# Kernel optimization log

Hardware: AMD Instinct MI355X
Metric: run time of the kernel (lower is better)

The kernel has to match this reference:

```python
import jax, jax.numpy as jnp
import numpy as np

N_NODES, EMB, HID, HEADS, E = 50000, 128, 64, 3, 800000


def setup_inputs() -> dict:
    key = jax.random.key(0)
    ks = jax.random.split(key, 12)
    HC = HEADS * HID
    return {
        "edge_index": jax.random.randint(ks[0], (2, E), 0, N_NODES),
        "edge_attr": jax.random.uniform(ks[1], (E, 1), dtype=jnp.float32),
        "path_emb": jax.random.normal(ks[2], (N_NODES, EMB), dtype=jnp.float32) * (2.0 / EMB) ** 0.5,
        "sim_w": jnp.ones((1,), dtype=jnp.float32),
        "Wl": jax.random.normal(ks[3], (HC, EMB), dtype=jnp.float32) / np.sqrt(EMB),
        "bl": jnp.zeros((HC,), dtype=jnp.float32),
        "Wr": jax.random.normal(ks[4], (HC, EMB), dtype=jnp.float32) / np.sqrt(EMB),
        "br": jnp.zeros((HC,), dtype=jnp.float32),
        "We": jax.random.normal(ks[5], (HC, 1), dtype=jnp.float32),
        "att": jax.random.normal(ks[6], (1, HEADS, HID), dtype=jnp.float32) / np.sqrt(HID),
        "bias_gnn": jnp.zeros((HID,), dtype=jnp.float32),
        "Wout": jax.random.normal(ks[7], (1, HID), dtype=jnp.float32) / np.sqrt(HID),
        "bout": jnp.zeros((1,), dtype=jnp.float32),
    }


def reference(edge_index, edge_attr, path_emb, sim_w, Wl, bl, Wr, br, We, att, bias_gnn, Wout, bout):
    # SimFusionModule: softmax-weighted combination over sim channels -> [E, 1]
    w = jax.nn.softmax(sim_w, axis=0)
    fused = (edge_attr * w).sum(axis=1, keepdims=True)  # [E,1]

    # GATv2Conv (concat=False, no self loops, edge_dim=1)
    xl = (path_emb @ Wl.T + bl).reshape(-1, HEADS, HID)  # source transform [N,H,C]
    xr = (path_emb @ Wr.T + br).reshape(-1, HEADS, HID)  # target transform [N,H,C]
    src, dst = edge_index[0], edge_index[1]
    xj = xl[src]                                          # [E,H,C] gathered source
    xi = xr[dst]                                          # [E,H,C] gathered target
    ef = (fused @ We.T).reshape(-1, HEADS, HID)           # [E,H,C] edge features
    m = xj + xi + ef
    a = (jax.nn.leaky_relu(m, 0.2) * att).sum(-1)         # [E,H] attention logits

    # segment softmax over incoming edges of each destination node
    amax = jax.ops.segment_max(a, dst, num_segments=N_NODES)
    aexp = jnp.exp(a - amax[dst])
    asum = jax.ops.segment_sum(aexp, dst, num_segments=N_NODES)
    alpha = aexp / asum[dst]                              # [E,H]

    out = jax.ops.segment_sum(alpha[:, :, None] * xj, dst, num_segments=N_NODES)  # [N,H,C]
    out = out.mean(axis=1) + bias_gnn                     # concat=False -> head mean, + bias

    scores = (out @ Wout.T + bout).squeeze()              # [N]
    return jax.nn.softmax(scores, axis=0)
```

## Files before the change

### kernel.cpp

```cpp
#include <hip/hip_runtime.h>
#include <cfloat>
#include <cmath>

#define NHEADS 3
#define HIDC   64
#define HCC    192
#define EMBC   128
#define WCOLS  384
#define CAP    1280

typedef unsigned short bhalf;
typedef __attribute__((ext_vector_type(8))) short bf16x8;
typedef __attribute__((ext_vector_type(4))) float f32x4;
typedef __attribute__((ext_vector_type(2))) float f32x2;

__device__ __forceinline__ unsigned f2bf(float f) {
  unsigned u = __float_as_uint(f);
  return (u + 0x7FFFu + ((u >> 16) & 1u)) >> 16;
}

__global__ __launch_bounds__(256) void prep_kernel(
    const float* __restrict__ Wl, const float* __restrict__ Wr,
    const float* __restrict__ bl, const float* __restrict__ br,
    const float* __restrict__ Wout, const float* __restrict__ We,
    const float* __restrict__ att,
    bhalf* __restrict__ Wb, float* __restrict__ vh, float* __restrict__ b16,
    float* __restrict__ We16, float* __restrict__ att16, float* __restrict__ ch,
    unsigned* __restrict__ cur, float* __restrict__ sumexp, int NB)
{
  const int BASE = WCOLS * EMBC;
  int gt = blockIdx.x * 256 + threadIdx.x;
  if (gt < BASE) {
    int c = gt >> 7, k = gt & 127;
    float v = (c < HCC) ? Wl[c * EMBC + k] : Wr[(c - HCC) * EMBC + k];
    Wb[gt] = (bhalf)f2bf(v);
  } else if (gt < BASE + 384) {
    int i = gt - BASE;
    int h = i >> 7, k = i & 127;
    float s = 0.f;
    for (int c = 0; c < HIDC; ++c)
      s += Wout[c] * Wl[(h * HIDC + c) * EMBC + k];
    vh[i] = s;
  } else if (gt < BASE + 768) {
    int c = gt - BASE - 384;
    b16[c] = 16.f * ((c < HCC) ? bl[c] : br[c - HCC]);
  } else if (gt < BASE + 960) {
    int c = gt - BASE - 768;
    We16[c] = 16.f * We[c];
  } else if (gt < BASE + 1152) {
    int c = gt - BASE - 960;
    att16[c] = att[c] * (1.f / 16.f);
  } else if (gt < BASE + 1155) {
    int h = gt - BASE - 1152;
    float s = 0.f;
    for (int c = 0; c < HIDC; ++c) s += bl[h * HIDC + c] * Wout[c];
    ch[h] = s;
  } else if (gt < BASE + 1155 + NB) {
    int b = gt - BASE - 1155;
    cur[b * 16] = (unsigned)(b * CAP);
  } else if (gt == BASE + 1155 + NB) {
    *sumexp = 0.f;
  }
}

__global__ __launch_bounds__(256, 4) void gemm_kernel(
    const float* __restrict__ pe, const bhalf* __restrict__ Wb,
    const float* __restrict__ b16, const float* __restrict__ vh,
    const float* __restrict__ ch,
    unsigned char* __restrict__ xl8, unsigned char* __restrict__ xr8,
    float* __restrict__ pj, int N)
{
  __shared__ bhalf Ws[192 * 64];
  const int tid  = threadIdx.x;
  const int w    = tid >> 6;
  const int lane = tid & 63;
  const int m    = lane & 15;
  const int q    = lane >> 4;
  const int nb   = blockIdx.x >> 1;
  const int half = blockIdx.x & 1;
  const int n0   = nb * 64;
  const int node = n0 + w * 16 + m;
  const size_t prow = (size_t)(node < N ? node : N - 1) * EMBC;

  bf16x8 pfrag[4];
  float pjp[3] = {0.f, 0.f, 0.f};
  #pragma unroll
  for (int kt = 0; kt < 4; ++kt) {
    const float* p = pe + prow + kt * 32 + q * 8;
    float4 x = *(const float4*)p;
    float4 y = *(const float4*)(p + 4);
    if (half == 0) {
      #pragma unroll
      for (int h = 0; h < 3; ++h) {
        const float* v = vh + h * EMBC + kt * 32 + q * 8;
        float4 va = *(const float4*)v;
        float4 vb = *(const float4*)(v + 4);
        pjp[h] += x.x*va.x + x.y*va.y + x.z*va.z + x.w*va.w
                + y.x*vb.x + y.y*vb.y + y.z*vb.z + y.w*vb.w;
      }
    }
    union { bf16x8 v; unsigned u[4]; } uu;
    uu.u[0] = (__float_as_uint(x.x) >> 16) | (__float_as_uint(x.y) & 0xFFFF0000u);
    uu.u[1] = (__float_as_uint(x.z) >> 16) | (__float_as_uint(x.w) & 0xFFFF0000u);
    uu.u[2] = (__float_as_uint(y.x) >> 16) | (__float_as_uint(y.y) & 0xFFFF0000u);
    uu.u[3] = (__float_as_uint(y.z) >> 16) | (__float_as_uint(y.w) & 0xFFFF0000u);
    pfrag[kt] = uu.v;
  }

  f32x4 acc[12];
  #pragma unroll
  for (int t = 0; t < 12; ++t) acc[t] = (f32x4){0.f, 0.f, 0.f, 0.f};

  for (int kh = 0; kh < 2; ++kh) {
    __syncthreads();
    for (int f = tid; f < 192 * 8; f += 256) {
      int cc = f >> 3, s = f & 7;
      uint4 v = *(const uint4*)(Wb + (size_t)(half * HCC + cc) * EMBC + kh * 64 + s * 8);
      *(uint4*)(Ws + cc * 64 + ((s ^ (cc & 7)) * 8)) = v;
    }
    __syncthreads();
    #pragma unroll
    for (int kt2 = 0; kt2 < 2; ++kt2) {
      #pragma unroll
      for (int t = 0; t < 12; ++t) {
        bf16x8 wf = *(const bf16x8*)(Ws + (t * 16 + m) * 64 + (((kt2 << 2) + q) ^ (m & 7)) * 8);
        acc[t] = __builtin_amdgcn_mfma_f32_16x16x32_bf16(wf, pfrag[kh * 2 + kt2], acc[t], 0, 0, 0);
      }
    }
  }

  if (half == 0) {
    #pragma unroll
    for (int h = 0; h < 3; ++h) {
      pjp[h] += __shfl_xor(pjp[h], 16);
      pjp[h] += __shfl_xor(pjp[h], 32);
    }
    if (q == 0 && node < N) {
      pj[node * 3 + 0] = pjp[0] + ch[0];
      pj[node * 3 + 1] = pjp[1] + ch[1];
      pj[node * 3 + 2] = pjp[2] + ch[2];
    }
  }

  if (node < N) {
    unsigned char* xo = half ? xr8 : xl8;
    #pragma unroll
    for (int t = 0; t < 12; ++t) {
      int col = t * 16 + q * 4;
      float4 b = *(const float4*)(b16 + half * HCC + col);
      float r0 = fmaf(acc[t][0], 16.f, b.x);
      float r1 = fmaf(acc[t][1], 16.f, b.y);
      float r2 = fmaf(acc[t][2], 16.f, b.z);
      float r3 = fmaf(acc[t][3], 16.f, b.w);
      int p = 0;
      p = __builtin_amdgcn_cvt_pk_fp8_f32(r0, r1, p, false);
      p = __builtin_amdgcn_cvt_pk_fp8_f32(r2, r3, p, true);
      *(unsigned*)(xo + (size_t)node * HCC + col) = (unsigned)p;
    }
  }
}

#define SCH 4096
__global__ __launch_bounds__(256) void scatter_kernel(
    const int* __restrict__ ei, const float* __restrict__ ea,
    uint2* __restrict__ eb, unsigned* __restrict__ cur, int E, int NB)
{
  __shared__ unsigned lh[800], lbase[800];
  int tid = threadIdx.x;
  int base = blockIdx.x * SCH;
  for (int i = tid; i < NB; i += 256) lh[i] = 0;
  __syncthreads();
  #pragma unroll 4
  for (int i = 0; i < SCH / 256; ++i) {
    int e = base + i * 256 + tid;
    if (e < E) atomicAdd(&lh[ei[E + e] >> 6], 1u);
  }
  __syncthreads();
  for (int i = tid; i < NB; i += 256) {
    unsigned c = lh[i];
    lbase[i] = c ? atomicAdd(&cur[i * 16], c) : 0u;
    lh[i] = 0;
  }
  __syncthreads();
  #pragma unroll 4
  for (int i = 0; i < SCH / 256; ++i) {
    int e = base + i * 256 + tid;
    if (e < E) {
      int src = ei[e], dst = ei[E + e];
      int bin = dst >> 6;
      unsigned slot = lbase[bin] + atomicAdd(&lh[bin], 1u);
      uint2 rec;
      rec.x = (unsigned)src | ((unsigned)dst << 16);
      rec.y = __float_as_uint(ea[e]);
      eb[slot] = rec;
    }
  }
}

#define EPG 5
#define GPW 4
#define WCHUNK (EPG * GPW)
__global__ __launch_bounds__(512, 4) void edge_kernel(
    const uint2* __restrict__ eb,
    const unsigned char* __restrict__ xl8, const unsigned char* __restrict__ xr8,
    const float* __restrict__ pj, const float* __restrict__ We16,
    const float* __restrict__ att16, const unsigned* __restrict__ cur,
    float* __restrict__ sumexp, float* __restrict__ out, int N)
{
  __shared__ uint4 xrs[64][12];
  __shared__ float facc[64][8];
  const int tid  = threadIdx.x;
  const int w    = tid >> 6;
  const int lane = tid & 63;
  const int j = lane / 12;
  const int c = lane % 12;
  const bool act = lane < 60;
  const int b = blockIdx.x;
  const int n0 = b << 6;
  const int start = b * CAP;
  const int end   = (int)cur[b * 16];

  for (int i = tid; i < 768; i += 512) {
    int row = i / 12, sl = i % 12;
    int nn = n0 + row; if (nn >= N) nn = N - 1;
    xrs[row][sl] = *(const uint4*)(xr8 + (size_t)nn * HCC + sl * 16);
  }
  for (int i = tid; i < 512; i += 512) ((float*)facc)[i] = 0.f;

  float4 we[4], at[4];
  #pragma unroll
  for (int i = 0; i < 4; ++i) {
    we[i] = *(const float4*)(We16 + c * 16 + i * 4);
    at[i] = *(const float4*)(att16 + c * 16 + i * 4);
  }
  __syncthreads();

  const int wstart = start + w * WCHUNK;
  uint2 rec[GPW];
  #pragma unroll
  for (int g = 0; g < GPW; ++g) {
    int e = wstart + g * EPG + j;
    rec[g] = eb[e < end ? e : start];
  }

  for (int cb = wstart; cb < end; cb += 8 * WCHUNK) {
    int srcs[GPW], dsts[GPW]; float eavs[GPW];
    #pragma unroll
    for (int g = 0; g < GPW; ++g) {
      srcs[g] = (int)(rec[g].x & 0xFFFFu);
      dsts[g] = (int)(rec[g].x >> 16);
      eavs[g] = __uint_as_float(rec[g].y);
    }
    uint4 ul[GPW]; float pjv[GPW];
    #pragma unroll
    for (int g = 0; g < GPW; ++g)
      ul[g] = *(const uint4*)(xl8 + (size_t)srcs[g] * HCC + c * 16);
    #pragma unroll
    for (int g = 0; g < GPW; ++g)
      pjv[g] = pj[srcs[g] * 3 + (c >> 2)];
    uint4 ur[GPW];
    #pragma unroll
    for (int g = 0; g < GPW; ++g)
      ur[g] = xrs[dsts[g] & 63][c];

    int nxt = cb + 8 * WCHUNK;
    #pragma unroll
    for (int g = 0; g < GPW; ++g) {
      int e = nxt + g * EPG + j;
      rec[g] = eb[(e < end) ? e : start];
    }

    #pragma unroll
    for (int g = 0; g < GPW; ++g) {
      const unsigned* ulp = &ul[g].x;
      const unsigned* urp = &ur[g].x;
      float sc = 0.f;
      #pragma unroll
      for (int i = 0; i < 4; ++i) {
        f32x2 l0 = __builtin_amdgcn_cvt_pk_f32_fp8(ulp[i], false);
        f32x2 l1 = __builtin_amdgcn_cvt_pk_f32_fp8(ulp[i], true);
        f32x2 r0 = __builtin_amdgcn_cvt_pk_f32_fp8(urp[i], false);
        f32x2 r1 = __builtin_amdgcn_cvt_pk_f32_fp8(urp[i], true);
        float m0 = l0.x + r0.x + eavs[g] * we[i].x;
        float m1 = l0.y + r0.y + eavs[g] * we[i].y;
        float m2 = l1.x + r1.x + eavs[g] * we[i].z;
        float m3 = l1.y + r1.y + eavs[g] * we[i].w;
        sc += fmaxf(m0, 0.2f * m0) * at[i].x
            + fmaxf(m1, 0.2f * m1) * at[i].y
            + fmaxf(m2, 0.2f * m2) * at[i].z
            + fmaxf(m3, 0.2f * m3) * at[i].w;
      }
      sc += __shfl_xor(sc, 1);
      sc += __shfl_xor(sc, 2);
      bool ve = act && (cb + g * EPG + j < end);
      if (ve && (c & 3) == 0) {
        int h = c >> 2;
        int ld = dsts[g] & 63;
        float ex = __expf(sc);
        atomicAdd(&facc[ld][h], ex);
        atomicAdd(&facc[ld][3 + h], ex * pjv[g]);
      }
    }
  }
  __syncthreads();

  if (tid < 64) {
    int n = n0 + tid;
    float e = 0.f;
    if (n < N) {
      float accs = 0.f;
      #pragma unroll
      for (int h = 0; h < 3; ++h) {
        float d = facc[tid][h];
        if (d > 0.f) accs += facc[tid][3 + h] / d;
      }
      e = expf(accs * (1.f / 3.f));
      out[n] = e;
    }
    #pragma unroll
    for (int o = 32; o; o >>= 1) e += __shfl_xor(e, o);
    if (tid == 0) atomicAdd(sumexp, e);
  }
}

__global__ __launch_bounds__(256) void norm_kernel(
    float* __restrict__ out, const float* __restrict__ sumexp, int N)
{
  int n = blockIdx.x * 256 + threadIdx.x;
  if (n < N) out[n] /= *sumexp;
}

extern "C" void kernel_launch(void* const* d_in, const int* in_sizes, int n_in,
                              void* d_out, int out_size, void* d_ws, size_t ws_size,
                              hipStream_t stream) {
  const int*   ei   = (const int*)  d_in[0];
  const float* ea   = (const float*)d_in[1];
  const float* pe   = (const float*)d_in[2];
  const float* Wl   = (const float*)d_in[4];
  const float* bl   = (const float*)d_in[5];
  const float* Wr   = (const float*)d_in[6];
  const float* br   = (const float*)d_in[7];
  const float* We   = (const float*)d_in[8];
  const float* att  = (const float*)d_in[9];
  const float* Wout = (const float*)d_in[11];

  const int E = in_sizes[0] / 2;
  const int N = in_sizes[2] / EMBC;
  const int NB = (N + 63) >> 6;
  float* out = (float*)d_out;

  float* ws       = (float*)d_ws;
  float* sumexp   = ws;
  unsigned* cur   = (unsigned*)(ws + 16);
  float* pj       = ws + 16 + (size_t)NB * 16;
  float* vh       = pj + (size_t)3 * N;
  float* b16      = vh + 384;
  float* We16     = b16 + 384;
  float* att16    = We16 + 192;
  float* ch       = att16 + 192;
  bhalf* Wb       = (bhalf*)(ch + 16);
  unsigned char* xl8 = (unsigned char*)(Wb + (size_t)WCOLS * EMBC);
  unsigned char* xr8 = xl8 + (size_t)N * HCC;
  uint2* eb       = (uint2*)(xr8 + (size_t)N * HCC);

  const int BASE = WCOLS * EMBC;
  prep_kernel  <<<(BASE + 1155 + NB + 1 + 255) / 256, 256, 0, stream>>>(
      Wl, Wr, bl, br, Wout, We, att, Wb, vh, b16, We16, att16, ch,
      cur, sumexp, NB);
  gemm_kernel  <<<NB * 2, 256, 0, stream>>>(pe, Wb, b16, vh, ch, xl8, xr8, pj, N);
  scatter_kernel<<<(E + SCH - 1) / SCH, 256, 0, stream>>>(ei, ea, eb, cur, E, NB);
  edge_kernel  <<<NB, 512, 0, stream>>>(eb, xl8, xr8, pj, We16, att16, cur,
                                        sumexp, out, N);
  norm_kernel  <<<(N + 255) / 256, 256, 0, stream>>>(out, sumexp, N);
}
```

Baseline: 204.5 us.

## Split each destination bucket across four edge blocks with separate finalize kernel

The edge kernel now launches four 256-thread blocks per 64-node bucket instead of one 512-thread block, with each block handling an interleaved slice of the bucket's edges. Each block writes its partial shared-memory accumulators to global memory, and a new finalize kernel sums the partials, computes node scores and accumulates the softmax denominator. This is meant to raise occupancy and parallelism over the ~782 buckets. The cost is that every block reloads the xr tile, there is extra global traffic for partials, and one more launch. Other changes: the shared xr tile is padded to 13 columns to avoid bank conflicts, and the scatter chunk shrinks to 1024 edges so more blocks run.

```diff
diff --git a/kernel.cpp b/kernel.cpp
--- a/kernel.cpp
+++ b/kernel.cpp
@@ -8,6 +8,7 @@
 #define EMBC   128
 #define WCOLS  384
 #define CAP    1280
+#define SPLIT  4
 
 typedef unsigned short bhalf;
 typedef __attribute__((ext_vector_type(8))) short bf16x8;
@@ -160,7 +161,7 @@
   }
 }
 
-#define SCH 4096
+#define SCH 1024
 __global__ __launch_bounds__(256) void scatter_kernel(
     const int* __restrict__ ei, const float* __restrict__ ea,
     uint2* __restrict__ eb, unsigned* __restrict__ cur, int E, int NB)
@@ -200,14 +201,14 @@
 #define EPG 5
 #define GPW 4
 #define WCHUNK (EPG * GPW)
-__global__ __launch_bounds__(512, 4) void edge_kernel(
+__global__ __launch_bounds__(256, 4) void edge_kernel(
     const uint2* __restrict__ eb,
     const unsigned char* __restrict__ xl8, const unsigned char* __restrict__ xr8,
     const float* __restrict__ pj, const float* __restrict__ We16,
     const float* __restrict__ att16, const unsigned* __restrict__ cur,
-    float* __restrict__ sumexp, float* __restrict__ out, int N)
-{
-  __shared__ uint4 xrs[64][12];
+    float* __restrict__ pfacc, int N)
+{
+  __shared__ uint4 xrs[64][13];
   __shared__ float facc[64][8];
   const int tid  = threadIdx.x;
   const int w    = tid >> 6;
@@ -215,17 +216,19 @@
   const int j = lane / 12;
   const int c = lane % 12;
   const bool act = lane < 60;
-  const int b = blockIdx.x;
-  const int n0 = b << 6;
-  const int start = b * CAP;
-  const int end   = (int)cur[b * 16];
-
-  for (int i = tid; i < 768; i += 512) {
-    int row = i / 12, sl = i % 12;
+  const int blk    = blockIdx.x;
+  const int bucket = blk >> 2;
+  const int sl     = blk & 3;
+  const int n0 = bucket << 6;
+  const int start = bucket * CAP;
+  const int end   = (int)cur[bucket * 16];
+
+  for (int i = tid; i < 768; i += 256) {
+    int row = i / 12, slot = i % 12;
     int nn = n0 + row; if (nn >= N) nn = N - 1;
-    xrs[row][sl] = *(const uint4*)(xr8 + (size_t)nn * HCC + sl * 16);
-  }
-  for (int i = tid; i < 512; i += 512) ((float*)facc)[i] = 0.f;
+    xrs[row][slot] = *(const uint4*)(xr8 + (size_t)nn * HCC + slot * 16);
+  }
+  for (int i = tid; i < 512; i += 256) ((float*)facc)[i] = 0.f;
 
   float4 we[4], at[4];
   #pragma unroll
@@ -235,7 +238,8 @@
   }
   __syncthreads();
 
-  const int wstart = start + w * WCHUNK;
+  const int gw = sl * 4 + w;
+  const int wstart = start + gw * WCHUNK;
   uint2 rec[GPW];
   #pragma unroll
   for (int g = 0; g < GPW; ++g) {
@@ -243,7 +247,7 @@
     rec[g] = eb[e < end ? e : start];
   }
 
-  for (int cb = wstart; cb < end; cb += 8 * WCHUNK) {
+  for (int cb = wstart; cb < end; cb += 16 * WCHUNK) {
     int srcs[GPW], dsts[GPW]; float eavs[GPW];
     #pragma unroll
     for (int g = 0; g < GPW; ++g) {
@@ -263,7 +267,7 @@
     for (int g = 0; g < GPW; ++g)
       ur[g] = xrs[dsts[g] & 63][c];
 
-    int nxt = cb + 8 * WCHUNK;
+    int nxt = cb + 16 * WCHUNK;
     #pragma unroll
     for (int g = 0; g < GPW; ++g) {
       int e = nxt + g * EPG + j;
@@ -304,23 +308,41 @@
   }
   __syncthreads();
 
-  if (tid < 64) {
-    int n = n0 + tid;
-    float e = 0.f;
-    if (n < N) {
-      float accs = 0.f;
-      #pragma unroll
-      for (int h = 0; h < 3; ++h) {
-        float d = facc[tid][h];
-        if (d > 0.f) accs += facc[tid][3 + h] / d;
-      }
-      e = expf(accs * (1.f / 3.f));
-      out[n] = e;
-    }
-    #pragma unroll
-    for (int o = 32; o; o >>= 1) e += __shfl_xor(e, o);
-    if (tid == 0) atomicAdd(sumexp, e);
-  }
+  for (int i = tid; i < 512; i += 256)
+    pfacc[(size_t)blk * 512 + i] = ((float*)facc)[i];
+}
+
+__global__ __launch_bounds__(256) void finalize_kernel(
+    const float* __restrict__ pfacc, float* __restrict__ sumexp,
+    float* __restrict__ out, int N)
+{
+  int n = blockIdx.x * 256 + threadIdx.x;
+  int t = threadIdx.x;
+  float e = 0.f;
+  if (n < N) {
+    int bucket = n >> 6, ld = n & 63;
+    float a0 = 0.f, a1 = 0.f, a2 = 0.f, m0 = 0.f, m1 = 0.f, m2 = 0.f;
+    #pragma unroll
+    for (int s = 0; s < SPLIT; ++s) {
+      const float* p = pfacc + ((size_t)(bucket * SPLIT + s) * 512) + ld * 8;
+      a0 += p[0]; a1 += p[1]; a2 += p[2];
+      m0 += p[3]; m1 += p[4]; m2 += p[5];
+    }
+    float accs = 0.f;
+    if (a0 > 0.f) accs += m0 / a0;
+    if (a1 > 0.f) accs += m1 / a1;
+    if (a2 > 0.f) accs += m2 / a2;
+    e = expf(accs * (1.f / 3.f));
+    out[n] = e;
+  }
+  __shared__ float red[256];
+  red[t] = e;
+  __syncthreads();
+  for (int w = 128; w; w >>= 1) {
+    if (t < w) red[t] += red[t + w];
+    __syncthreads();
+  }
+  if (t == 0) atomicAdd(sumexp, red[0]);
 }
 
 __global__ __launch_bounds__(256) void norm_kernel(
@@ -356,12 +378,13 @@
   float* vh       = pj + (size_t)3 * N;
   float* b16      = vh + 384;
   float* We16     = b16 + 384;
-  float* att16    = We16 + 192;
+  float* att16   = We16 + 192;
   float* ch       = att16 + 192;
   bhalf* Wb       = (bhalf*)(ch + 16);
   unsigned char* xl8 = (unsigned char*)(Wb + (size_t)WCOLS * EMBC);
   unsigned char* xr8 = xl8 + (size_t)N * HCC;
   uint2* eb       = (uint2*)(xr8 + (size_t)N * HCC);
+  float* pfacc    = (float*)(eb + (size_t)NB * CAP);
 
   const int BASE = WCOLS * EMBC;
   prep_kernel  <<<(BASE + 1155 + NB + 1 + 255) / 256, 256, 0, stream>>>(
@@ -369,7 +392,8 @@
       cur, sumexp, NB);
   gemm_kernel  <<<NB * 2, 256, 0, stream>>>(pe, Wb, b16, vh, ch, xl8, xr8, pj, N);
   scatter_kernel<<<(E + SCH - 1) / SCH, 256, 0, stream>>>(ei, ea, eb, cur, E, NB);
-  edge_kernel  <<<NB, 512, 0, stream>>>(eb, xl8, xr8, pj, We16, att16, cur,
-                                        sumexp, out, N);
+  edge_kernel  <<<NB * SPLIT, 256, 0, stream>>>(eb, xl8, xr8, pj, We16, att16,
+                                                cur, pfacc, N);
+  finalize_kernel<<<(N + 255) / 256, 256, 0, stream>>>(pfacc, sumexp, out, N);
   norm_kernel  <<<(N + 255) / 256, 256, 0, stream>>>(out, sumexp, N);
 }
```

After: 229.5 us. 1.12x slower.

## Store node features as fp16, use packed fp16 math, fuse gemm with scatter

Applied to the files above, without the earlier changes.

Replaces the fp8-with-scaling storage of the projected node features with fp16 and rewrites the edge attention loop to use packed half2 adds, max and fdot2. The gemm and edge-bucketing scatter kernels are merged into one launch, with blocks chosen by index and LDS shared through a union. The aim is to cut conversion instructions and one launch, and to let the gemm and scatter work overlap. In exchange, the source feature gathers and the xr tile in LDS are twice as large, which adds memory traffic in the gather-bound edge kernel.

```diff
diff --git a/kernel.cpp b/kernel.cpp
--- a/kernel.cpp
+++ b/kernel.cpp
@@ -8,15 +8,20 @@
 #define EMBC   128
 #define WCOLS  384
 #define CAP    1280
+#define SCH    4096
 
 typedef unsigned short bhalf;
+typedef __fp16 half_t;
+typedef __attribute__((ext_vector_type(2))) __fp16 h2;
 typedef __attribute__((ext_vector_type(8))) short bf16x8;
 typedef __attribute__((ext_vector_type(4))) float f32x4;
-typedef __attribute__((ext_vector_type(2))) float f32x2;
 
 __device__ __forceinline__ unsigned f2bf(float f) {
   unsigned u = __float_as_uint(f);
   return (u + 0x7FFFu + ((u >> 16) & 1u)) >> 16;
+}
+__device__ __forceinline__ unsigned h2bits(h2 v) {
+  union { h2 h; unsigned u; } cv; cv.h = v; return cv.u;
 }
 
 __global__ __launch_bounds__(256) void prep_kernel(
@@ -24,9 +29,10 @@
     const float* __restrict__ bl, const float* __restrict__ br,
     const float* __restrict__ Wout, const float* __restrict__ We,
     const float* __restrict__ att,
-    bhalf* __restrict__ Wb, float* __restrict__ vh, float* __restrict__ b16,
-    float* __restrict__ We16, float* __restrict__ att16, float* __restrict__ ch,
-    unsigned* __restrict__ cur, float* __restrict__ sumexp, int NB)
+    bhalf* __restrict__ Wb, float* __restrict__ vh, float* __restrict__ bfl,
+    unsigned* __restrict__ weh, unsigned* __restrict__ atth,
+    float* __restrict__ ch, unsigned* __restrict__ cur,
+    float* __restrict__ sumexp, int NB)
 {
   const int BASE = WCOLS * EMBC;
   int gt = blockIdx.x * 256 + threadIdx.x;
@@ -43,156 +49,151 @@
     vh[i] = s;
   } else if (gt < BASE + 768) {
     int c = gt - BASE - 384;
-    b16[c] = 16.f * ((c < HCC) ? bl[c] : br[c - HCC]);
+    bfl[c] = (c < HCC) ? bl[c] : br[c - HCC];
+  } else if (gt < BASE + 864) {
+    int i = gt - BASE - 768;
+    weh[i] = h2bits(__builtin_amdgcn_cvt_pkrtz(We[2 * i], We[2 * i + 1]));
   } else if (gt < BASE + 960) {
-    int c = gt - BASE - 768;
-    We16[c] = 16.f * We[c];
-  } else if (gt < BASE + 1152) {
-    int c = gt - BASE - 960;
-    att16[c] = att[c] * (1.f / 16.f);
-  } else if (gt < BASE + 1155) {
-    int h = gt - BASE - 1152;
+    int i = gt - BASE - 864;
+    atth[i] = h2bits(__builtin_amdgcn_cvt_pkrtz(att[2 * i], att[2 * i + 1]));
+  } else if (gt < BASE + 963) {
+    int h = gt - BASE - 960;
     float s = 0.f;
     for (int c = 0; c < HIDC; ++c) s += bl[h * HIDC + c] * Wout[c];
     ch[h] = s;
-  } else if (gt < BASE + 1155 + NB) {
-    int b = gt - BASE - 1155;
+  } else if (gt < BASE + 963 + NB) {
+    int b = gt - BASE - 963;
     cur[b * 16] = (unsigned)(b * CAP);
-  } else if (gt == BASE + 1155 + NB) {
+  } else if (gt == BASE + 963 + NB) {
     *sumexp = 0.f;
   }
 }
 
-__global__ __launch_bounds__(256, 4) void gemm_kernel(
+__global__ __launch_bounds__(256, 4) void gemmscatter_kernel(
     const float* __restrict__ pe, const bhalf* __restrict__ Wb,
-    const float* __restrict__ b16, const float* __restrict__ vh,
+    const float* __restrict__ bfl, const float* __restrict__ vh,
     const float* __restrict__ ch,
-    unsigned char* __restrict__ xl8, unsigned char* __restrict__ xr8,
-    float* __restrict__ pj, int N)
+    half_t* __restrict__ xlh, half_t* __restrict__ xrh,
+    float* __restrict__ pj, int N,
+    const int* __restrict__ ei, const float* __restrict__ ea,
+    uint2* __restrict__ eb, unsigned* __restrict__ cur, int E, int NB2)
 {
-  __shared__ bhalf Ws[192 * 64];
-  const int tid  = threadIdx.x;
-  const int w    = tid >> 6;
-  const int lane = tid & 63;
-  const int m    = lane & 15;
-  const int q    = lane >> 4;
-  const int nb   = blockIdx.x >> 1;
-  const int half = blockIdx.x & 1;
-  const int n0   = nb * 64;
-  const int node = n0 + w * 16 + m;
-  const size_t prow = (size_t)(node < N ? node : N - 1) * EMBC;
-
-  bf16x8 pfrag[4];
-  float pjp[3] = {0.f, 0.f, 0.f};
-  #pragma unroll
-  for (int kt = 0; kt < 4; ++kt) {
-    const float* p = pe + prow + kt * 32 + q * 8;
-    float4 x = *(const float4*)p;
-    float4 y = *(const float4*)(p + 4);
+  __shared__ union {
+    bhalf Ws[192 * 64];
+    struct { unsigned lh[800]; unsigned lbase[800]; } s;
+  } sm;
+  const int tid = threadIdx.x;
+
+  if ((int)blockIdx.x < NB2) {
+    const int w    = tid >> 6;
+    const int lane = tid & 63;
+    const int m    = lane & 15;
+    const int q    = lane >> 4;
+    const int nb   = blockIdx.x >> 1;
+    const int half = blockIdx.x & 1;
+    const int node = nb * 64 + w * 16 + m;
+    const size_t prow = (size_t)(node < N ? node : N - 1) * EMBC;
+
+    bf16x8 pfrag[4];
+    float pjp[3] = {0.f, 0.f, 0.f};
+    #pragma unroll
+    for (int kt = 0; kt < 4; ++kt) {
+      const float* p = pe + prow + kt * 32 + q * 8;
+      float4 x = *(const float4*)p;
+      float4 y = *(const float4*)(p + 4);
+      if (half == 0) {
+        #pragma unroll
+        for (int h = 0; h < 3; ++h) {
+          const float* v = vh + h * EMBC + kt * 32 + q * 8;
+          float4 va = *(const float4*)v;
+          float4 vb = *(const float4*)(v + 4);
+          pjp[h] += x.x*va.x + x.y*va.y + x.z*va.z + x.w*va.w
+                  + y.x*vb.x + y.y*vb.y + y.z*vb.z + y.w*vb.w;
+        }
+      }
+      union { bf16x8 v; unsigned u[4]; } uu;
+      uu.u[0] = (__float_as_uint(x.x) >> 16) | (__float_as_uint(x.y) & 0xFFFF0000u);
+      uu.u[1] = (__float_as_uint(x.z) >> 16) | (__float_as_uint(x.w) & 0xFFFF0000u);
+      uu.u[2] = (__float_as_uint(y.x) >> 16) | (__float_as_uint(y.y) & 0xFFFF0000u);
+      uu.u[3] = (__float_as_uint(y.z) >> 16) | (__float_as_uint(y.w) & 0xFFFF0000u);
+      pfrag[kt] = uu.v;
+    }
+
+    f32x4 acc[12];
+    #pragma unroll
+    for (int t = 0; t < 12; ++t) acc[t] = (f32x4){0.f, 0.f, 0.f, 0.f};
+
+    for (int kh = 0; kh < 2; ++kh) {
+      __syncthreads();
+      for (int f = tid; f < 192 * 8; f += 256) {
+        int cc = f >> 3, s = f & 7;
+        uint4 v = *(const uint4*)(Wb + (size_t)(half * HCC + cc) * EMBC + kh * 64 + s * 8);
+        *(uint4*)(sm.Ws + cc * 64 + ((s ^ (cc & 7)) * 8)) = v;
+      }
+      __syncthreads();
+      #pragma unroll
+      for (int kt2 = 0; kt2 < 2; ++kt2) {
+        #pragma unroll
+        for (int t = 0; t < 12; ++t) {
+          bf16x8 wf = *(const bf16x8*)(sm.Ws + (t * 16 + m) * 64 + (((kt2 << 2) + q) ^ (m & 7)) * 8);
+          acc[t] = __builtin_amdgcn_mfma_f32_16x16x32_bf16(wf, pfrag[kh * 2 + kt2], acc[t], 0, 0, 0);
+        }
+      }
+    }
+
     if (half == 0) {
       #pragma unroll
       for (int h = 0; h < 3; ++h) {
-        const float* v = vh + h * EMBC + kt * 32 + q * 8;
-        float4 va = *(const float4*)v;
-        float4 vb = *(const float4*)(v + 4);
-        pjp[h] += x.x*va.x + x.y*va.y + x.z*va.z + x.w*va.w
-                + y.x*vb.x + y.y*vb.y + y.z*vb.z + y.w*vb.w;
-      }
-    }
-    union { bf16x8 v; unsigned u[4]; } uu;
-    uu.u[0] = (__float_as_uint(x.x) >> 16) | (__float_as_uint(x.y) & 0xFFFF0000u);
-    uu.u[1] = (__float_as_uint(x.z) >> 16) | (__float_as_uint(x.w) & 0xFFFF0000u);
-    uu.u[2] = (__float_as_uint(y.x) >> 16) | (__float_as_uint(y.y) & 0xFFFF0000u);
-    uu.u[3] = (__float_as_uint(y.z) >> 16) | (__float_as_uint(y.w) & 0xFFFF0000u);
-    pfrag[kt] = uu.v;
-  }
-
-  f32x4 acc[12];
-  #pragma unroll
-  for (int t = 0; t < 12; ++t) acc[t] = (f32x4){0.f, 0.f, 0.f, 0.f};
-
-  for (int kh = 0; kh < 2; ++kh) {
+        pjp[h] += __shfl_xor(pjp[h], 16);
+        pjp[h] += __shfl_xor(pjp[h], 32);
+      }
+      if (q == 0 && node < N) {
+        pj[node * 3 + 0] = pjp[0] + ch[0];
+        pj[node * 3 + 1] = pjp[1] + ch[1];
+        pj[node * 3 + 2] = pjp[2] + ch[2];
+      }
+    }
+
+    if (node < N) {
+      half_t* xo = half ? xrh : xlh;
+      #pragma unroll
+      for (int t = 0; t < 12; ++t) {
+        int col = t * 16 + q * 4;
+        float4 b = *(const float4*)(bfl + half * HCC + col);
+        h2 pa = __builtin_amdgcn_cvt_pkrtz(acc[t][0] + b.x, acc[t][1] + b.y);
+        h2 pb = __builtin_amdgcn_cvt_pkrtz(acc[t][2] + b.z, acc[t][3] + b.w);
+        uint2 st; st.x = h2bits(pa); st.y = h2bits(pb);
+        *(uint2*)(xo + (size_t)node * HCC + col) = st;
+      }
+    }
+  } else {
+    const int base = (blockIdx.x - NB2) * SCH;
+    for (int i = tid; i < 800; i += 256) sm.s.lh[i] = 0;
     __syncthreads();
-    for (int f = tid; f < 192 * 8; f += 256) {
-      int cc = f >> 3, s = f & 7;
-      uint4 v = *(const uint4*)(Wb + (size_t)(half * HCC + cc) * EMBC + kh * 64 + s * 8);
-      *(uint4*)(Ws + cc * 64 + ((s ^ (cc & 7)) * 8)) = v;
+    #pragma unroll 4
+    for (int i = 0; i < SCH / 256; ++i) {
+      int e = base + i * 256 + tid;
+      if (e < E) atomicAdd(&sm.s.lh[ei[E + e] >> 6], 1u);
     }
     __syncthreads();
-    #pragma unroll
-    for (int kt2 = 0; kt2 < 2; ++kt2) {
-      #pragma unroll
-      for (int t = 0; t < 12; ++t) {
-        bf16x8 wf = *(const bf16x8*)(Ws + (t * 16 + m) * 64 + (((kt2 << 2) + q) ^ (m & 7)) * 8);
-        acc[t] = __builtin_amdgcn_mfma_f32_16x16x32_bf16(wf, pfrag[kh * 2 + kt2], acc[t], 0, 0, 0);
-      }
-    }
-  }
-
-  if (half == 0) {
-    #pragma unroll
-    for (int h = 0; h < 3; ++h) {
-      pjp[h] += __shfl_xor(pjp[h], 16);
-      pjp[h] += __shfl_xor(pjp[h], 32);
-    }
-    if (q == 0 && node < N) {
-      pj[node * 3 + 0] = pjp[0] + ch[0];
-      pj[node * 3 + 1] = pjp[1] + ch[1];
-      pj[node * 3 + 2] = pjp[2] + ch[2];
-    }
-  }
-
-  if (node < N) {
-    unsigned char* xo = half ? xr8 : xl8;
-    #pragma unroll
-    for (int t = 0; t < 12; ++t) {
-      int col = t * 16 + q * 4;
-      float4 b = *(const float4*)(b16 + half * HCC + col);
-      float r0 = fmaf(acc[t][0], 16.f, b.x);
-      float r1 = fmaf(acc[t][1], 16.f, b.y);
-      float r2 = fmaf(acc[t][2], 16.f, b.z);
-      float r3 = fmaf(acc[t][3], 16.f, b.w);
-      int p = 0;
-      p = __builtin_amdgcn_cvt_pk_fp8_f32(r0, r1, p, false);
-      p = __builtin_amdgcn_cvt_pk_fp8_f32(r2, r3, p, true);
-      *(unsigned*)(xo + (size_t)node * HCC + col) = (unsigned)p;
-    }
-  }
-}
-
-#define SCH 4096
-__global__ __launch_bounds__(256) void scatter_kernel(
-    const int* __restrict__ ei, const float* __restrict__ ea,
-    uint2* __restrict__ eb, unsigned* __restrict__ cur, int E, int NB)
-{
-  __shared__ unsigned lh[800], lbase[800];
-  int tid = threadIdx.x;
-  int base = blockIdx.x * SCH;
-  for (int i = tid; i < NB; i += 256) lh[i] = 0;
-  __syncthreads();
-  #pragma unroll 4
-  for (int i = 0; i < SCH / 256; ++i) {
-    int e = base + i * 256 + tid;
-    if (e < E) atomicAdd(&lh[ei[E + e] >> 6], 1u);
-  }
-  __syncthreads();
-  for (int i = tid; i < NB; i += 256) {
-    unsigned c = lh[i];
-    lbase[i] = c ? atomicAdd(&cur[i * 16], c) : 0u;
-    lh[i] = 0;
-  }
-  __syncthreads();
-  #pragma unroll 4
-  for (int i = 0; i < SCH / 256; ++i) {
-    int e = base + i * 256 + tid;
-    if (e < E) {
-      int src = ei[e], dst = ei[E + e];
-      int bin = dst >> 6;
-      unsigned slot = lbase[bin] + atomicAdd(&lh[bin], 1u);
-      uint2 rec;
-      rec.x = (unsigned)src | ((unsigned)dst << 16);
-      rec.y = __float_as_uint(ea[e]);
-      eb[slot] = rec;
+    for (int i = tid; i < 800; i += 256) {
+      unsigned c = sm.s.lh[i];
+      sm.s.lbase[i] = c ? atomicAdd(&cur[i * 16], c) : 0u;
+      sm.s.lh[i] = 0;
+    }
+    __syncthreads();
+    #pragma unroll 4
+    for (int i = 0; i < SCH / 256; ++i) {
+      int e = base + i * 256 + tid;
+      if (e < E) {
+        int src = ei[e], dst = ei[E + e];
+        int bin = dst >> 6;
+        unsigned slot = sm.s.lbase[bin] + atomicAdd(&sm.s.lh[bin], 1u);
+        uint2 rec;
+        rec.x = (unsigned)src | ((unsigned)dst << 16);
+        rec.y = __float_as_uint(ea[e]);
+        eb[slot] = rec;
+      }
     }
   }
 }
@@ -202,12 +203,12 @@
 #define WCHUNK (EPG * GPW)
 __global__ __launch_bounds__(512, 4) void edge_kernel(
     const uint2* __restrict__ eb,
-    const unsigned char* __restrict__ xl8, const unsigned char* __restrict__ xr8,
-    const float* __restrict__ pj, const float* __restrict__ We16,
-    const float* __restrict__ att16, const unsigned* __restrict__ cur,
+    const half_t* __restrict__ xlh, const half_t* __restrict__ xrh,
+    const float* __restrict__ pj, const unsigned* __restrict__ weh,
+    const unsigned* __restrict__ atth, const unsigned* __restrict__ cur,
     float* __restrict__ sumexp, float* __restrict__ out, int N)
 {
-  __shared__ uint4 xrs[64][12];
+  __shared__ uint4 xrs[64][25];
   __shared__ float facc[64][8];
   const int tid  = threadIdx.x;
   const int w    = tid >> 6;
@@ -220,19 +221,20 @@
   const int start = b * CAP;
   const int end   = (int)cur[b * 16];
 
-  for (int i = tid; i < 768; i += 512) {
-    int row = i / 12, sl = i % 12;
+  for (int i = tid; i < 64 * 24; i += 512) {
+    int row = i / 24, sl = i % 24;
     int nn = n0 + row; if (nn >= N) nn = N - 1;
-    xrs[row][sl] = *(const uint4*)(xr8 + (size_t)nn * HCC + sl * 16);
-  }
-  for (int i = tid; i < 512; i += 512) ((float*)facc)[i] = 0.f;
-
-  float4 we[4], at[4];
-  #pragma unroll
-  for (int i = 0; i < 4; ++i) {
-    we[i] = *(const float4*)(We16 + c * 16 + i * 4);
-    at[i] = *(const float4*)(att16 + c * 16 + i * 4);
-  }
+    xrs[row][sl] = *(const uint4*)(xrh + (size_t)nn * HCC + sl * 8);
+  }
+  if (tid < 512) ((float*)facc)[tid] = 0.f;
+
+  union U8 { uint4 u[2]; h2 h[8]; };
+  U8 we, at;
+  we.u[0] = *(const uint4*)(weh + c * 8);
+  we.u[1] = *(const uint4*)(weh + c * 8 + 4);
+  at.u[0] = *(const uint4*)(atth + c * 8);
+  at.u[1] = *(const uint4*)(atth + c * 8 + 4);
+  const h2 c02 = {(__fp16)0.2f, (__fp16)0.2f};
   __syncthreads();
 
   const int wstart = start + w * WCHUNK;
@@ -251,17 +253,17 @@
       dsts[g] = (int)(rec[g].x >> 16);
       eavs[g] = __uint_as_float(rec[g].y);
     }
-    uint4 ul[GPW]; float pjv[GPW];
-    #pragma unroll
-    for (int g = 0; g < GPW; ++g)
-      ul[g] = *(const uint4*)(xl8 + (size_t)srcs[g] * HCC + c * 16);
+    union U8x { uint4 u[2]; h2 h[8]; };
+    U8x ul[GPW]; float pjv[GPW];
+    #pragma unroll
+    for (int g = 0; g < GPW; ++g) {
+      const half_t* rp = xlh + (size_t)srcs[g] * HCC + c * 16;
+      ul[g].u[0] = ((const uint4*)rp)[0];
+      ul[g].u[1] = ((const uint4*)rp)[1];
+    }
     #pragma unroll
     for (int g = 0; g < GPW; ++g)
       pjv[g] = pj[srcs[g] * 3 + (c >> 2)];
-    uint4 ur[GPW];
-    #pragma unroll
-    for (int g = 0; g < GPW; ++g)
-      ur[g] = xrs[dsts[g] & 63][c];
 
     int nxt = cb + 8 * WCHUNK;
     #pragma unroll
@@ -272,30 +274,23 @@
 
     #pragma unroll
     for (int g = 0; g < GPW; ++g) {
-      const unsigned* ulp = &ul[g].x;
-      const unsigned* urp = &ur[g].x;
+      int ld = dsts[g] & 63;
+      U8x ur;
+      ur.u[0] = xrs[ld][c * 2];
+      ur.u[1] = xrs[ld][c * 2 + 1];
+      h2 eav2 = __builtin_amdgcn_cvt_pkrtz(eavs[g], eavs[g]);
       float sc = 0.f;
       #pragma unroll
-      for (int i = 0; i < 4; ++i) {
-        f32x2 l0 = __builtin_amdgcn_cvt_pk_f32_fp8(ulp[i], false);
-        f32x2 l1 = __builtin_amdgcn_cvt_pk_f32_fp8(ulp[i], true);
-        f32x2 r0 = __builtin_amdgcn_cvt_pk_f32_fp8(urp[i], false);
-        f32x2 r1 = __builtin_amdgcn_cvt_pk_f32_fp8(urp[i], true);
-        float m0 = l0.x + r0.x + eavs[g] * we[i].x;
-        float m1 = l0.y + r0.y + eavs[g] * we[i].y;
-        float m2 = l1.x + r1.x + eavs[g] * we[i].z;
-        float m3 = l1.y + r1.y + eavs[g] * we[i].w;
-        sc += fmaxf(m0, 0.2f * m0) * at[i].x
-            + fmaxf(m1, 0.2f * m1) * at[i].y
-            + fmaxf(m2, 0.2f * m2) * at[i].z
-            + fmaxf(m3, 0.2f * m3) * at[i].w;
+      for (int i = 0; i < 8; ++i) {
+        h2 m  = ul[g].h[i] + ur.h[i] + eav2 * we.h[i];
+        h2 lr = __builtin_elementwise_max(m, m * c02);
+        sc = __builtin_amdgcn_fdot2(lr, at.h[i], sc, false);
       }
       sc += __shfl_xor(sc, 1);
       sc += __shfl_xor(sc, 2);
       bool ve = act && (cb + g * EPG + j < end);
       if (ve && (c & 3) == 0) {
         int h = c >> 2;
-        int ld = dsts[g] & 63;
         float ex = __expf(sc);
         atomicAdd(&facc[ld][h], ex);
         atomicAdd(&facc[ld][3 + h], ex * pjv[g]);
@@ -354,22 +349,24 @@
   unsigned* cur   = (unsigned*)(ws + 16);
   float* pj       = ws + 16 + (size_t)NB * 16;
   float* vh       = pj + (size_t)3 * N;
-  float* b16      = vh + 384;
-  float* We16     = b16 + 384;
-  float* att16    = We16 + 192;
-  float* ch       = att16 + 192;
+  float* bfl      = vh + 384;
+  unsigned* weh   = (unsigned*)(bfl + 384);
+  unsigned* atth  = weh + 96;
+  float* ch       = (float*)(atth + 96);
   bhalf* Wb       = (bhalf*)(ch + 16);
-  unsigned char* xl8 = (unsigned char*)(Wb + (size_t)WCOLS * EMBC);
-  unsigned char* xr8 = xl8 + (size_t)N * HCC;
-  uint2* eb       = (uint2*)(xr8 + (size_t)N * HCC);
+  half_t* xlh     = (half_t*)(Wb + (size_t)WCOLS * EMBC);
+  half_t* xrh     = xlh + (size_t)N * HCC;
+  uint2* eb       = (uint2*)(xrh + (size_t)N * HCC);
 
   const int BASE = WCOLS * EMBC;
-  prep_kernel  <<<(BASE + 1155 + NB + 1 + 255) / 256, 256, 0, stream>>>(
-      Wl, Wr, bl, br, Wout, We, att, Wb, vh, b16, We16, att16, ch,
+  const int NB2 = NB * 2;
+  const int NSC = (E + SCH - 1) / SCH;
+  prep_kernel<<<(BASE + 963 + NB + 1 + 255) / 256, 256, 0, stream>>>(
+      Wl, Wr, bl, br, Wout, We, att, Wb, vh, bfl, weh, atth, ch,
       cur, sumexp, NB);
-  gemm_kernel  <<<NB * 2, 256, 0, stream>>>(pe, Wb, b16, vh, ch, xl8, xr8, pj, N);
-  scatter_kernel<<<(E + SCH - 1) / SCH, 256, 0, stream>>>(ei, ea, eb, cur, E, NB);
-  edge_kernel  <<<NB, 512, 0, stream>>>(eb, xl8, xr8, pj, We16, att16, cur,
-                                        sumexp, out, N);
-  norm_kernel  <<<(N + 255) / 256, 256, 0, stream>>>(out, sumexp, N);
-}
+  gemmscatter_kernel<<<NB2 + NSC, 256, 0, stream>>>(
+      pe, Wb, bfl, vh, ch, xlh, xrh, pj, N, ei, ea, eb, cur, E, NB2);
+  edge_kernel<<<NB, 512, 0, stream>>>(eb, xlh, xrh, pj, weh, atth, cur,
+                                      sumexp, out, N);
+  norm_kernel<<<(N + 255) / 256, 256, 0, stream>>>(out, sumexp, N);
+}
```

After: 211.9 us. 1.04x slower.
